# Kernel optimization log

Measured on AMD Instinct MI355X. Metric: run time of the kernel, lower is better.

The kernel has to match this reference:

```python
import jax, jax.numpy as jnp
import numpy as np

TEMPERATURE = 0.5


def setup_inputs() -> dict:
    key = jax.random.key(0)
    k1, k2 = jax.random.split(key)
    emb = jax.random.normal(k1, (16384, 128), dtype=jnp.float32)
    emb = emb / jnp.linalg.norm(emb, axis=1, keepdims=True)  # L2-normalized, per docstring
    labels = jax.random.randint(k2, (16384,), 0, 64, dtype=jnp.int64)
    return {"embeddings": emb, "partition_labels": labels}


def reference(embeddings, partition_labels):
    n = embeddings.shape[0]
    # [N, N] similarity matrix, scaled by temperature
    sim = jnp.matmul(embeddings, embeddings.T) / TEMPERATURE
    exp_sim = jnp.exp(sim)
    eye = jnp.eye(n, dtype=bool)
    pos_mask = (partition_labels[None, :] == partition_labels[:, None]) & ~eye
    # numerator: sum of exp over positives; denominator: sum over all k != i
    pos_sum = jnp.sum(jnp.where(pos_mask, exp_sim, 0.0), axis=1)
    all_sum = jnp.sum(jnp.where(~eye, exp_sim, 0.0), axis=1)
    valid = jnp.any(pos_mask, axis=1)
    loss_i = -(jnp.log(pos_sum) - jnp.log(all_sum))
    n_valid = jnp.sum(valid)
    total = jnp.sum(jnp.where(valid, loss_i, 0.0))
    return jnp.where(n_valid > 0, total / n_valid, 0.0)
```

## Files before the change

### kernel.cpp

```cpp
#include <hip/hip_runtime.h>

#define N_EMB 16384
#define DIM 128
#define NSPLIT 16
#define CPS (N_EMB / NSPLIT)
#define BN 64
#define NCT (CPS / BN)
#define NLAB 64
#define POSY 4

typedef __bf16 bf16x8 __attribute__((ext_vector_type(8)));
typedef float f32x4 __attribute__((ext_vector_type(4)));
typedef unsigned short us8 __attribute__((ext_vector_type(8)));
typedef unsigned int u32;

#define SCALE 2.8853900817779268f
#define LN2 0.6931471805599453f

__device__ inline float fast_exp2(float x) {
#if __has_builtin(__builtin_amdgcn_exp2f)
  return __builtin_amdgcn_exp2f(x);
#else
  return exp2f(x);
#endif
}
__device__ inline float fast_log2(float x) {
#if __has_builtin(__builtin_amdgcn_logf)
  return __builtin_amdgcn_logf(x);
#else
  return log2f(x);
#endif
}

__device__ inline unsigned short f2bf(float f) {
  unsigned int u = __float_as_uint(f);
  u += 0x7fffu + ((u >> 16) & 1u);
  return (unsigned short)(u >> 16);
}

__device__ inline void gll16(const unsigned short* g, unsigned short* l) {
  __builtin_amdgcn_global_load_lds(
      (const __attribute__((address_space(1))) u32*)g,
      (__attribute__((address_space(3))) u32*)l, 16, 0, 0);
}

__global__ __launch_bounds__(1024) void perm_kernel(
    const int* __restrict__ labels, int* __restrict__ perm,
    int* __restrict__ gstart) {
  __shared__ int whist[16][NLAB];
  __shared__ int htot[NLAB];
  const int tid = threadIdx.x;
  const int w = tid >> 6, lane = tid & 63;
  whist[w][lane] = 0;
  __syncthreads();
  const int base_i = w * 1024;
  int mylab[16];
#pragma unroll
  for (int k = 0; k < 16; ++k) {
    int lab = labels[base_i + k * 64 + lane];
    mylab[k] = lab;
    atomicAdd(&whist[w][lab], 1);
  }
  __syncthreads();
  if (tid < NLAB) {
    int s = 0;
#pragma unroll
    for (int ww = 0; ww < 16; ++ww) {
      int t = whist[ww][tid];
      whist[ww][tid] = s;
      s += t;
    }
    htot[tid] = s;
  }
  __syncthreads();
  if (tid == 0) {
    int s = 0;
    for (int l = 0; l < NLAB; ++l) {
      int t = htot[l];
      gstart[l] = s;
      htot[l] = s;
      s += t;
    }
    gstart[NLAB] = s;
  }
  __syncthreads();
  whist[w][lane] += htot[lane];
  __syncthreads();
#pragma unroll
  for (int k = 0; k < 16; ++k) {
    int lab = mylab[k];
    int pos = atomicAdd(&whist[w][lab], 1);
    perm[pos] = base_i + k * 64 + lane;
  }
}

__global__ __launch_bounds__(256) void preconv(
    const float* __restrict__ emb, const int* __restrict__ perm,
    unsigned short* __restrict__ eraw) {
  const int tid = threadIdx.x;
  const int tile = blockIdx.x >> 2;
  const int part = blockIdx.x & 3;
  const size_t base = (size_t)tile * (128 * DIM);
#pragma unroll
  for (int i = 0; i < 2; ++i) {
    int G = part * 512 + i * 256 + tid;
    int col16 = G & 15;
    int qd = (G >> 4) & 3;
    int ks = (G >> 6) & 3;
    int tc = G >> 8;
    int srow = perm[tile * 128 + tc * 16 + col16];
    const float* p = emb + (size_t)srow * DIM + ks * 32 + qd * 8;
    float4 a = *reinterpret_cast<const float4*>(p);
    float4 b = *reinterpret_cast<const float4*>(p + 4);
    us8 g;
    g[0] = f2bf(a.x); g[1] = f2bf(a.y); g[2] = f2bf(a.z); g[3] = f2bf(a.w);
    g[4] = f2bf(b.x); g[5] = f2bf(b.y); g[6] = f2bf(b.z); g[7] = f2bf(b.w);
    *reinterpret_cast<us8*>(eraw + base + (size_t)G * 8) = g;
  }
}

__device__ inline bf16x8 load_scaled(const unsigned short* p) {
  us8 v = *reinterpret_cast<const us8*>(p);
  us8 s;
#pragma unroll
  for (int j = 0; j < 8; ++j)
    s[j] = f2bf(__uint_as_float((u32)v[j] << 16) * SCALE);
  return *reinterpret_cast<bf16x8*>(&s);
}

__global__ __launch_bounds__(128) void cl_fused(
    const unsigned short* __restrict__ eraw, const int* __restrict__ gstart,
    float* __restrict__ ws_all, float* __restrict__ ws_pos,
    float* __restrict__ ws_diag) {
  __shared__ unsigned short lds0[BN * DIM];
  __shared__ unsigned short lds1[BN * DIM];
  const int tid = threadIdx.x;
  const int lane = tid & 63;
  const int w = tid >> 6;
  const int col16 = lane & 15;
  const int quad = lane >> 4;
  const int cs = blockIdx.y;

  if (cs < NSPLIT) {
    const int r0 = blockIdx.x * 128;

    bf16x8 afrag[4][4];
#pragma unroll
    for (int tr = 0; tr < 4; ++tr) {
      const int T = (r0 >> 4) + w * 4 + tr;
      const unsigned short* p = eraw + (size_t)(T >> 3) * (128 * DIM) +
                                ((T & 7) * 4) * 512 + lane * 8;
#pragma unroll
      for (int ks = 0; ks < 4; ++ks) afrag[tr][ks] = load_scaled(p + ks * 512);
    }

    float all_p[16];
#pragma unroll
    for (int t = 0; t < 16; ++t) all_p[t] = 0.f;

    auto stage = [&](unsigned short* dst, int c0) {
      const unsigned short* g = eraw + (size_t)(c0 >> 7) * (128 * DIM) +
                                (size_t)((c0 >> 6) & 1) * 8192;
#pragma unroll
      for (int i = 0; i < 8; ++i) {
        int chunk = i * 2 + w;
        gll16(g + chunk * 512 + lane * 8, dst + chunk * 512);
      }
    };
    auto computeB = [&](const unsigned short* buf) {
#pragma unroll
      for (int tc = 0; tc < 4; ++tc) {
        bf16x8 bfr[4];
#pragma unroll
        for (int ks = 0; ks < 4; ++ks)
          bfr[ks] = *reinterpret_cast<const bf16x8*>(buf + (tc * 4 + ks) * 512 +
                                                     lane * 8);
#pragma unroll
        for (int tr = 0; tr < 4; ++tr) {
          f32x4 acc = {0.f, 0.f, 0.f, 0.f};
#pragma unroll
          for (int ks = 0; ks < 4; ++ks)
            acc = __builtin_amdgcn_mfma_f32_16x16x32_bf16(afrag[tr][ks],
                                                          bfr[ks], acc, 0, 0, 0);
#pragma unroll
          for (int r = 0; r < 4; ++r) all_p[tr * 4 + r] += fast_exp2(acc[r]);
        }
      }
    };

    const int cbase = cs * CPS;
    stage(lds0, cbase);
    __syncthreads();
    for (int ct = 0; ct < NCT; ct += 2) {
      if (ct + 1 < NCT) stage(lds1, cbase + (ct + 1) * BN);
      computeB(lds0);
      __syncthreads();
      if (ct + 2 < NCT) stage(lds0, cbase + (ct + 2) * BN);
      computeB(lds1);
      __syncthreads();
    }

#pragma unroll
    for (int t = 0; t < 16; ++t) {
      float a = all_p[t];
#pragma unroll
      for (int m = 8; m >= 1; m >>= 1) a += __shfl_xor(a, m, 64);
      if (col16 == 0) {
        int row_g = r0 + w * 64 + (t >> 2) * 16 + quad * 4 + (t & 3);
        ws_all[cs * N_EMB + row_g] = a;
      }
    }
  } else {
    const int l = blockIdx.x >> 1;
    const int chunk = (cs - NSPLIT) * 2 + (blockIdx.x & 1);
    const int gs = gstart[l], ge = gstart[l + 1];
    const int t0 = gs >> 4;
    const int t1 = (ge + 15) >> 4;

    for (int ta = t0 + chunk * 2 + w; ta < t1; ta += 16) {
      bf16x8 af[4];
      const unsigned short* pa = eraw + (size_t)(ta >> 3) * (128 * DIM) +
                                 ((ta & 7) * 4) * 512 + lane * 8;
#pragma unroll
      for (int ks = 0; ks < 4; ++ks) af[ks] = load_scaled(pa + ks * 512);
      const int grow = ta * 16 + quad * 4;
      float posr[4] = {0.f, 0.f, 0.f, 0.f};

      for (int tb = t0; tb < t1; ++tb) {
        bf16x8 bfr[4];
        const unsigned short* pb = eraw + (size_t)(tb >> 3) * (128 * DIM) +
                                   ((tb & 7) * 4) * 512 + lane * 8;
#pragma unroll
        for (int ks = 0; ks < 4; ++ks)
          bfr[ks] = *reinterpret_cast<const bf16x8*>(pb + ks * 512);
        f32x4 acc = {0.f, 0.f, 0.f, 0.f};
#pragma unroll
        for (int ks = 0; ks < 4; ++ks)
          acc = __builtin_amdgcn_mfma_f32_16x16x32_bf16(af[ks], bfr[ks], acc,
                                                        0, 0, 0);
        const int gcol = tb * 16 + col16;
        const bool colin = (gcol >= gs) && (gcol < ge);
#pragma unroll
        for (int r = 0; r < 4; ++r) {
          float e = fast_exp2(acc[r]);
          const int gr = grow + r;
          if (gcol == gr) {
            if (colin) ws_diag[gr] = e;
          } else if (colin) {
            posr[r] += e;
          }
        }
      }

#pragma unroll
      for (int r = 0; r < 4; ++r) {
        float p = posr[r];
#pragma unroll
        for (int m = 8; m >= 1; m >>= 1) p += __shfl_xor(p, m, 64);
        const int gr = grow + r;
        if (col16 == 0 && gr >= gs && gr < ge) ws_pos[gr] = p;
      }
    }
  }
}

__global__ __launch_bounds__(256) void fin1(
    const float* __restrict__ ws_all, const float* __restrict__ ws_pos,
    const float* __restrict__ ws_diag, float* __restrict__ part_tot,
    int* __restrict__ part_cnt) {
  __shared__ float s_t[256];
  __shared__ int s_c[256];
  const int tid = threadIdx.x;
  const int row = blockIdx.x * 256 + tid;
  float a = 0.f;
#pragma unroll
  for (int s = 0; s < NSPLIT; ++s) a += ws_all[s * N_EMB + row];
  a -= ws_diag[row];
  const float p = ws_pos[row];
  float t = 0.f;
  int c = 0;
  if (p > 0.f) {
    t = fast_log2(a) - fast_log2(p);
    c = 1;
  }
  s_t[tid] = t;
  s_c[tid] = c;
  __syncthreads();
  for (int s = 128; s > 0; s >>= 1) {
    if (tid < s) {
      s_t[tid] += s_t[tid + s];
      s_c[tid] += s_c[tid + s];
    }
    __syncthreads();
  }
  if (tid == 0) {
    part_tot[blockIdx.x] = s_t[0];
    part_cnt[blockIdx.x] = s_c[0];
  }
}

__global__ __launch_bounds__(64) void fin2(const float* __restrict__ part_tot,
                                           const int* __restrict__ part_cnt,
                                           float* __restrict__ out) {
  const int tid = threadIdx.x;
  float t = part_tot[tid];
  int c = part_cnt[tid];
#pragma unroll
  for (int m = 32; m >= 1; m >>= 1) {
    t += __shfl_xor(t, m, 64);
    c += __shfl_xor(c, m, 64);
  }
  if (tid == 0) out[0] = (c > 0) ? (t * LN2 / (float)c) : 0.f;
}

extern "C" void kernel_launch(void* const* d_in, const int* in_sizes, int n_in,
                              void* d_out, int out_size, void* d_ws,
                              size_t ws_size, hipStream_t stream) {
  const float* emb = (const float*)d_in[0];
  const int* labels = (const int*)d_in[1];

  unsigned short* eraw = (unsigned short*)d_ws;
  float* ws_all = (float*)(eraw + (size_t)N_EMB * DIM);
  float* ws_pos = ws_all + NSPLIT * N_EMB;
  float* ws_diag = ws_pos + N_EMB;
  float* part_tot = ws_diag + N_EMB;
  int* part_cnt = (int*)(part_tot + 64);
  int* perm = part_cnt + 64;
  int* gstart = perm + N_EMB;

  perm_kernel<<<1, 1024, 0, stream>>>(labels, perm, gstart);
  preconv<<<512, 256, 0, stream>>>(emb, perm, eraw);
  cl_fused<<<dim3(128, NSPLIT + POSY), 128, 0, stream>>>(eraw, gstart, ws_all,
                                                         ws_pos, ws_diag);
  fin1<<<N_EMB / 256, 256, 0, stream>>>(ws_all, ws_pos, ws_diag, part_tot,
                                        part_cnt);
  fin2<<<1, 64, 0, stream>>>(part_tot, part_cnt, (float*)d_out);
}
```

Before: 155.9 us.

## Replace LDS-staged B tiles with direct register double-buffered global loads

The main similarity loop now drops the LDS double-buffer (global_load_lds plus block barriers) and has each wavefront load B fragments straight from global/L2 into registers, double-buffered in registers. Blocks grow to 256 threads with 64 rows per wave, and the positive-pair section is rearranged to one block per label with four waves. This removes barriers and LDS traffic, but every wave now fetches B data on its own, raising L2 load traffic and register pressure. The positive pass has less parallelism (64 blocks instead of 256).

```diff
diff --git a/kernel.cpp b/kernel.cpp
--- a/kernel.cpp
+++ b/kernel.cpp
@@ -4,10 +4,8 @@
 #define DIM 128
 #define NSPLIT 16
 #define CPS (N_EMB / NSPLIT)
-#define BN 64
-#define NCT (CPS / BN)
+#define TCOLS (CPS / 16)
 #define NLAB 64
-#define POSY 4
 
 typedef __bf16 bf16x8 __attribute__((ext_vector_type(8)));
 typedef float f32x4 __attribute__((ext_vector_type(4)));
@@ -36,12 +34,6 @@
   unsigned int u = __float_as_uint(f);
   u += 0x7fffu + ((u >> 16) & 1u);
   return (unsigned short)(u >> 16);
-}
-
-__device__ inline void gll16(const unsigned short* g, unsigned short* l) {
-  __builtin_amdgcn_global_load_lds(
-      (const __attribute__((address_space(1))) u32*)g,
-      (__attribute__((address_space(3))) u32*)l, 16, 0, 0);
 }
 
 __global__ __launch_bounds__(1024) void perm_kernel(
@@ -128,12 +120,20 @@
   return *reinterpret_cast<bf16x8*>(&s);
 }
 
-__global__ __launch_bounds__(128) void cl_fused(
+__device__ inline void loadB(bf16x8* dst,
+                             const unsigned short* __restrict__ eraw, int T,
+                             int lane) {
+  const unsigned short* p =
+      eraw + (size_t)(T >> 3) * (128 * DIM) + ((T & 7) * 4) * 512 + lane * 8;
+#pragma unroll
+  for (int ks = 0; ks < 4; ++ks)
+    dst[ks] = *reinterpret_cast<const bf16x8*>(p + ks * 512);
+}
+
+__global__ __launch_bounds__(256) void cl_fused(
     const unsigned short* __restrict__ eraw, const int* __restrict__ gstart,
     float* __restrict__ ws_all, float* __restrict__ ws_pos,
     float* __restrict__ ws_diag) {
-  __shared__ unsigned short lds0[BN * DIM];
-  __shared__ unsigned short lds1[BN * DIM];
   const int tid = threadIdx.x;
   const int lane = tid & 63;
   const int w = tid >> 6;
@@ -142,12 +142,12 @@
   const int cs = blockIdx.y;
 
   if (cs < NSPLIT) {
-    const int r0 = blockIdx.x * 128;
+    const int r0 = blockIdx.x * 256 + w * 64;
 
     bf16x8 afrag[4][4];
 #pragma unroll
     for (int tr = 0; tr < 4; ++tr) {
-      const int T = (r0 >> 4) + w * 4 + tr;
+      const int T = (r0 >> 4) + tr;
       const unsigned short* p = eraw + (size_t)(T >> 3) * (128 * DIM) +
                                 ((T & 7) * 4) * 512 + lane * 8;
 #pragma unroll
@@ -158,46 +158,27 @@
 #pragma unroll
     for (int t = 0; t < 16; ++t) all_p[t] = 0.f;
 
-    auto stage = [&](unsigned short* dst, int c0) {
-      const unsigned short* g = eraw + (size_t)(c0 >> 7) * (128 * DIM) +
-                                (size_t)((c0 >> 6) & 1) * 8192;
-#pragma unroll
-      for (int i = 0; i < 8; ++i) {
-        int chunk = i * 2 + w;
-        gll16(g + chunk * 512 + lane * 8, dst + chunk * 512);
+    auto compute = [&](const bf16x8* b) {
+#pragma unroll
+      for (int tr = 0; tr < 4; ++tr) {
+        f32x4 acc = {0.f, 0.f, 0.f, 0.f};
+#pragma unroll
+        for (int ks = 0; ks < 4; ++ks)
+          acc = __builtin_amdgcn_mfma_f32_16x16x32_bf16(afrag[tr][ks], b[ks],
+                                                        acc, 0, 0, 0);
+#pragma unroll
+        for (int r = 0; r < 4; ++r) all_p[tr * 4 + r] += fast_exp2(acc[r]);
       }
     };
-    auto computeB = [&](const unsigned short* buf) {
-#pragma unroll
-      for (int tc = 0; tc < 4; ++tc) {
-        bf16x8 bfr[4];
-#pragma unroll
-        for (int ks = 0; ks < 4; ++ks)
-          bfr[ks] = *reinterpret_cast<const bf16x8*>(buf + (tc * 4 + ks) * 512 +
-                                                     lane * 8);
-#pragma unroll
-        for (int tr = 0; tr < 4; ++tr) {
-          f32x4 acc = {0.f, 0.f, 0.f, 0.f};
-#pragma unroll
-          for (int ks = 0; ks < 4; ++ks)
-            acc = __builtin_amdgcn_mfma_f32_16x16x32_bf16(afrag[tr][ks],
-                                                          bfr[ks], acc, 0, 0, 0);
-#pragma unroll
-          for (int r = 0; r < 4; ++r) all_p[tr * 4 + r] += fast_exp2(acc[r]);
-        }
-      }
-    };
-
-    const int cbase = cs * CPS;
-    stage(lds0, cbase);
-    __syncthreads();
-    for (int ct = 0; ct < NCT; ct += 2) {
-      if (ct + 1 < NCT) stage(lds1, cbase + (ct + 1) * BN);
-      computeB(lds0);
-      __syncthreads();
-      if (ct + 2 < NCT) stage(lds0, cbase + (ct + 2) * BN);
-      computeB(lds1);
-      __syncthreads();
+
+    const int Tbase = cs * TCOLS;
+    bf16x8 b0[4], b1[4];
+    loadB(b0, eraw, Tbase, lane);
+    for (int ct = 0; ct < TCOLS; ct += 2) {
+      loadB(b1, eraw, Tbase + ct + 1, lane);
+      compute(b0);
+      if (ct + 2 < TCOLS) loadB(b0, eraw, Tbase + ct + 2, lane);
+      compute(b1);
     }
 
 #pragma unroll
@@ -206,18 +187,17 @@
 #pragma unroll
       for (int m = 8; m >= 1; m >>= 1) a += __shfl_xor(a, m, 64);
       if (col16 == 0) {
-        int row_g = r0 + w * 64 + (t >> 2) * 16 + quad * 4 + (t & 3);
+        int row_g = r0 + (t >> 2) * 16 + quad * 4 + (t & 3);
         ws_all[cs * N_EMB + row_g] = a;
       }
     }
   } else {
-    const int l = blockIdx.x >> 1;
-    const int chunk = (cs - NSPLIT) * 2 + (blockIdx.x & 1);
+    const int l = blockIdx.x;
     const int gs = gstart[l], ge = gstart[l + 1];
     const int t0 = gs >> 4;
     const int t1 = (ge + 15) >> 4;
 
-    for (int ta = t0 + chunk * 2 + w; ta < t1; ta += 16) {
+    for (int ta = t0 + w; ta < t1; ta += 4) {
       bf16x8 af[4];
       const unsigned short* pa = eraw + (size_t)(ta >> 3) * (128 * DIM) +
                                  ((ta & 7) * 4) * 512 + lane * 8;
@@ -228,11 +208,7 @@
 
       for (int tb = t0; tb < t1; ++tb) {
         bf16x8 bfr[4];
-        const unsigned short* pb = eraw + (size_t)(tb >> 3) * (128 * DIM) +
-                                   ((tb & 7) * 4) * 512 + lane * 8;
-#pragma unroll
-        for (int ks = 0; ks < 4; ++ks)
-          bfr[ks] = *reinterpret_cast<const bf16x8*>(pb + ks * 512);
+        loadB(bfr, eraw, tb, lane);
         f32x4 acc = {0.f, 0.f, 0.f, 0.f};
 #pragma unroll
         for (int ks = 0; ks < 4; ++ks)
@@ -330,8 +306,8 @@
 
   perm_kernel<<<1, 1024, 0, stream>>>(labels, perm, gstart);
   preconv<<<512, 256, 0, stream>>>(emb, perm, eraw);
-  cl_fused<<<dim3(128, NSPLIT + POSY), 128, 0, stream>>>(eraw, gstart, ws_all,
-                                                         ws_pos, ws_diag);
+  cl_fused<<<dim3(64, NSPLIT + 1), 256, 0, stream>>>(eraw, gstart, ws_all,
+                                                     ws_pos, ws_diag);
   fin1<<<N_EMB / 256, 256, 0, stream>>>(ws_all, ws_pos, ws_diag, part_tot,
                                         part_cnt);
   fin2<<<1, 64, 0, stream>>>(part_tot, part_cnt, (float*)d_out);
```

After: 182.6 us. 1.17x slower.

## Drop LDS double buffering, halve column splits, merge finalize kernels

Applied to the files above, without the earlier changes.

The all-pairs pass now uses 8 column splits with a single 128-column LDS tile, synchronized before and after each load, instead of double-buffered 64-column tiles across 16 splits. The positive-pair pass goes from four grid rows to one, with each block covering more row tiles. The two finalize kernels are merged into one 1024-thread block. This cuts the grid size and the number of launches, but it gives up the overlap of global-to-LDS loads with MFMA work and leaves fewer blocks to fill the GPU.

```diff
diff --git a/kernel.cpp b/kernel.cpp
--- a/kernel.cpp
+++ b/kernel.cpp
@@ -2,12 +2,11 @@
 
 #define N_EMB 16384
 #define DIM 128
-#define NSPLIT 16
+#define NSPLIT 8
 #define CPS (N_EMB / NSPLIT)
-#define BN 64
+#define BN 128
 #define NCT (CPS / BN)
 #define NLAB 64
-#define POSY 4
 
 typedef __bf16 bf16x8 __attribute__((ext_vector_type(8)));
 typedef float f32x4 __attribute__((ext_vector_type(4)));
@@ -128,12 +127,21 @@
   return *reinterpret_cast<bf16x8*>(&s);
 }
 
+__device__ inline void loadB(bf16x8* dst,
+                             const unsigned short* __restrict__ eraw, int T,
+                             int lane) {
+  const unsigned short* p =
+      eraw + (size_t)(T >> 3) * (128 * DIM) + ((T & 7) * 4) * 512 + lane * 8;
+#pragma unroll
+  for (int ks = 0; ks < 4; ++ks)
+    dst[ks] = *reinterpret_cast<const bf16x8*>(p + ks * 512);
+}
+
 __global__ __launch_bounds__(128) void cl_fused(
     const unsigned short* __restrict__ eraw, const int* __restrict__ gstart,
     float* __restrict__ ws_all, float* __restrict__ ws_pos,
     float* __restrict__ ws_diag) {
-  __shared__ unsigned short lds0[BN * DIM];
-  __shared__ unsigned short lds1[BN * DIM];
+  __shared__ unsigned short lds[BN * DIM];
   const int tid = threadIdx.x;
   const int lane = tid & 63;
   const int w = tid >> 6;
@@ -158,22 +166,25 @@
 #pragma unroll
     for (int t = 0; t < 16; ++t) all_p[t] = 0.f;
 
-    auto stage = [&](unsigned short* dst, int c0) {
-      const unsigned short* g = eraw + (size_t)(c0 >> 7) * (128 * DIM) +
-                                (size_t)((c0 >> 6) & 1) * 8192;
-#pragma unroll
-      for (int i = 0; i < 8; ++i) {
-        int chunk = i * 2 + w;
-        gll16(g + chunk * 512 + lane * 8, dst + chunk * 512);
-      }
-    };
-    auto computeB = [&](const unsigned short* buf) {
-#pragma unroll
-      for (int tc = 0; tc < 4; ++tc) {
+    for (int ct = 0; ct < NCT; ++ct) {
+      const int c0 = cs * CPS + ct * BN;
+      __syncthreads();
+      {
+        const unsigned short* g = eraw + (size_t)(c0 >> 7) * (128 * DIM);
+#pragma unroll
+        for (int i = 0; i < 16; ++i) {
+          int chunk = i * 2 + w;
+          gll16(g + chunk * 512 + lane * 8, lds + chunk * 512);
+        }
+      }
+      __syncthreads();
+
+#pragma unroll
+      for (int tc = 0; tc < 8; ++tc) {
         bf16x8 bfr[4];
 #pragma unroll
         for (int ks = 0; ks < 4; ++ks)
-          bfr[ks] = *reinterpret_cast<const bf16x8*>(buf + (tc * 4 + ks) * 512 +
+          bfr[ks] = *reinterpret_cast<const bf16x8*>(lds + (tc * 4 + ks) * 512 +
                                                      lane * 8);
 #pragma unroll
         for (int tr = 0; tr < 4; ++tr) {
@@ -181,23 +192,12 @@
 #pragma unroll
           for (int ks = 0; ks < 4; ++ks)
             acc = __builtin_amdgcn_mfma_f32_16x16x32_bf16(afrag[tr][ks],
-                                                          bfr[ks], acc, 0, 0, 0);
+                                                          bfr[ks], acc, 0, 0,
+                                                          0);
 #pragma unroll
           for (int r = 0; r < 4; ++r) all_p[tr * 4 + r] += fast_exp2(acc[r]);
         }
       }
-    };
-
-    const int cbase = cs * CPS;
-    stage(lds0, cbase);
-    __syncthreads();
-    for (int ct = 0; ct < NCT; ct += 2) {
-      if (ct + 1 < NCT) stage(lds1, cbase + (ct + 1) * BN);
-      computeB(lds0);
-      __syncthreads();
-      if (ct + 2 < NCT) stage(lds0, cbase + (ct + 2) * BN);
-      computeB(lds1);
-      __syncthreads();
     }
 
 #pragma unroll
@@ -212,12 +212,12 @@
     }
   } else {
     const int l = blockIdx.x >> 1;
-    const int chunk = (cs - NSPLIT) * 2 + (blockIdx.x & 1);
+    const int sub = blockIdx.x & 1;
     const int gs = gstart[l], ge = gstart[l + 1];
     const int t0 = gs >> 4;
     const int t1 = (ge + 15) >> 4;
 
-    for (int ta = t0 + chunk * 2 + w; ta < t1; ta += 16) {
+    for (int ta = t0 + sub * 2 + w; ta < t1; ta += 4) {
       bf16x8 af[4];
       const unsigned short* pa = eraw + (size_t)(ta >> 3) * (128 * DIM) +
                                  ((ta & 7) * 4) * 512 + lane * 8;
@@ -228,11 +228,7 @@
 
       for (int tb = t0; tb < t1; ++tb) {
         bf16x8 bfr[4];
-        const unsigned short* pb = eraw + (size_t)(tb >> 3) * (128 * DIM) +
-                                   ((tb & 7) * 4) * 512 + lane * 8;
-#pragma unroll
-        for (int ks = 0; ks < 4; ++ks)
-          bfr[ks] = *reinterpret_cast<const bf16x8*>(pb + ks * 512);
+        loadB(bfr, eraw, tb, lane);
         f32x4 acc = {0.f, 0.f, 0.f, 0.f};
 #pragma unroll
         for (int ks = 0; ks < 4; ++ks)
@@ -264,53 +260,38 @@
   }
 }
 
-__global__ __launch_bounds__(256) void fin1(
-    const float* __restrict__ ws_all, const float* __restrict__ ws_pos,
-    const float* __restrict__ ws_diag, float* __restrict__ part_tot,
-    int* __restrict__ part_cnt) {
-  __shared__ float s_t[256];
-  __shared__ int s_c[256];
+__global__ __launch_bounds__(1024) void fin(const float* __restrict__ ws_all,
+                                            const float* __restrict__ ws_pos,
+                                            const float* __restrict__ ws_diag,
+                                            float* __restrict__ out) {
+  __shared__ float s_t[1024];
+  __shared__ int s_c[1024];
   const int tid = threadIdx.x;
-  const int row = blockIdx.x * 256 + tid;
-  float a = 0.f;
-#pragma unroll
-  for (int s = 0; s < NSPLIT; ++s) a += ws_all[s * N_EMB + row];
-  a -= ws_diag[row];
-  const float p = ws_pos[row];
-  float t = 0.f;
-  int c = 0;
-  if (p > 0.f) {
-    t = fast_log2(a) - fast_log2(p);
-    c = 1;
-  }
-  s_t[tid] = t;
-  s_c[tid] = c;
-  __syncthreads();
-  for (int s = 128; s > 0; s >>= 1) {
+  float tot = 0.f;
+  int cnt = 0;
+  for (int row = tid; row < N_EMB; row += 1024) {
+    float a = 0.f;
+#pragma unroll
+    for (int s = 0; s < NSPLIT; ++s) a += ws_all[s * N_EMB + row];
+    a -= ws_diag[row];
+    const float p = ws_pos[row];
+    if (p > 0.f) {
+      tot += fast_log2(a) - fast_log2(p);
+      cnt++;
+    }
+  }
+  s_t[tid] = tot;
+  s_c[tid] = cnt;
+  __syncthreads();
+  for (int s = 512; s > 0; s >>= 1) {
     if (tid < s) {
       s_t[tid] += s_t[tid + s];
       s_c[tid] += s_c[tid + s];
     }
     __syncthreads();
   }
-  if (tid == 0) {
-    part_tot[blockIdx.x] = s_t[0];
-    part_cnt[blockIdx.x] = s_c[0];
-  }
-}
-
-__global__ __launch_bounds__(64) void fin2(const float* __restrict__ part_tot,
-                                           const int* __restrict__ part_cnt,
-                                           float* __restrict__ out) {
-  const int tid = threadIdx.x;
-  float t = part_tot[tid];
-  int c = part_cnt[tid];
-#pragma unroll
-  for (int m = 32; m >= 1; m >>= 1) {
-    t += __shfl_xor(t, m, 64);
-    c += __shfl_xor(c, m, 64);
-  }
-  if (tid == 0) out[0] = (c > 0) ? (t * LN2 / (float)c) : 0.f;
+  if (tid == 0)
+    out[0] = (s_c[0] > 0) ? (s_t[0] * LN2 / (float)s_c[0]) : 0.f;
 }
 
 extern "C" void kernel_launch(void* const* d_in, const int* in_sizes, int n_in,
@@ -323,16 +304,12 @@
   float* ws_all = (float*)(eraw + (size_t)N_EMB * DIM);
   float* ws_pos = ws_all + NSPLIT * N_EMB;
   float* ws_diag = ws_pos + N_EMB;
-  float* part_tot = ws_diag + N_EMB;
-  int* part_cnt = (int*)(part_tot + 64);
-  int* perm = part_cnt + 64;
+  int* perm = (int*)(ws_diag + N_EMB);
   int* gstart = perm + N_EMB;
 
   perm_kernel<<<1, 1024, 0, stream>>>(labels, perm, gstart);
   preconv<<<512, 256, 0, stream>>>(emb, perm, eraw);
-  cl_fused<<<dim3(128, NSPLIT + POSY), 128, 0, stream>>>(eraw, gstart, ws_all,
-                                                         ws_pos, ws_diag);
-  fin1<<<N_EMB / 256, 256, 0, stream>>>(ws_all, ws_pos, ws_diag, part_tot,
-                                        part_cnt);
-  fin2<<<1, 64, 0, stream>>>(part_tot, part_cnt, (float*)d_out);
-}
+  cl_fused<<<dim3(128, NSPLIT + 1), 128, 0, stream>>>(eraw, gstart, ws_all,
+                                                      ws_pos, ws_diag);
+  fin<<<1, 1024, 0, stream>>>(ws_all, ws_pos, ws_diag, (float*)d_out);
+}
```

Result: slower. 188.8 us (+21.1%).
